# Kernel optimization log

Measured on AMD Instinct MI355X. Metric: run time of the kernel, lower is better.

The kernel has to match this reference:

```python
import jax, jax.numpy as jnp
import numpy as np

# Static hyperparams matching init_kwargs
KSIZE, STRIDE, PAD, DIL = 3, 2, 1, 1


def setup_inputs() -> dict:
    key = jax.random.key(0)
    k1, k2 = jax.random.split(key)
    B, H, W, Cin, Cout = 8, 128, 128, 128, 256
    feats = jax.random.normal(k1, (B * H * W, Cin), dtype=jnp.float32)
    weight = jax.random.normal(k2, (KSIZE * KSIZE, Cin, Cout), dtype=jnp.float32) * 0.05
    alpha_upper = jnp.ones((1,), dtype=jnp.float32)
    # dense grid coords [N, 3] = (batch, y, x), matching a dense image sparse tensor
    bb, yy, xx = np.meshgrid(np.arange(B), np.arange(H), np.arange(W), indexing='ij')
    coords = jnp.asarray(np.stack([bb, yy, xx], -1).reshape(-1, 3), dtype=jnp.int32)
    return {"feats": feats, "weight": weight, "alpha_upper": alpha_upper,
            "coords": coords, "H": H, "W": W, "B": B}


def _coord_ranges(H, W):
    # Faithful translation of WrappedMinkowskiStridedOperation.__init__ + forward
    # coordinate math, specialized to a dense grid (per-batch min=0, max=H-1/W-1).
    kernel_origin = DIL * ((KSIZE - 1) // 2) * (KSIZE % 2)
    dilated = DIL * (KSIZE - 1) + 1
    ks_off = kernel_origin - dilated + 1          # _kernel_start_offset
    ke_off = kernel_origin                        # _kernel_end_offset
    idx_start = kernel_origin - PAD               # _index_start_offset
    ranges = []
    for ext in (H, W):
        idx_end = (ext - 1) + kernel_origin + PAD - dilated + 2
        start = max(idx_start, (0 + ks_off - idx_start) // STRIDE * STRIDE + idx_start)
        end = min(idx_end, ((ext - 1 + ke_off - idx_start) // STRIDE + 1) * STRIDE + idx_start)
        ranges.append(np.arange(start, end, STRIDE))
    offsets = np.arange(KSIZE) * DIL - kernel_origin  # kernel region offsets
    return ranges[0], ranges[1], offsets, idx_start


def reference(feats, weight, alpha_upper, coords, H, W, B):
    Cin = feats.shape[1]
    Cout = weight.shape[-1]
    ys, xs, offs, idx_start = _coord_ranges(H, W)
    OH, OW = len(ys), len(xs)
    oy, ox = jnp.meshgrid(jnp.asarray(ys, jnp.int32), jnp.asarray(xs, jnp.int32), indexing='ij')
    dy, dx = np.meshgrid(offs, offs, indexing='ij')
    dy = jnp.asarray(dy.reshape(-1), jnp.int32)  # [kvol]
    dx = jnp.asarray(dx.reshape(-1), jnp.int32)
    ny = oy[None] + dy[:, None, None]            # [kvol, OH, OW]
    nx = ox[None] + dx[:, None, None]
    valid = (ny >= 0) & (ny < H) & (nx >= 0) & (nx < W)
    lin = jnp.clip(ny, 0, H - 1) * W + jnp.clip(nx, 0, W - 1)  # [kvol, OH, OW]
    feats3 = feats.reshape(B, H * W, Cin)
    gathered = feats3[:, lin]                    # [B, kvol, OH, OW, Cin]
    gathered = jnp.where(valid[None, ..., None], gathered, jnp.zeros((), feats.dtype))
    out = jnp.einsum('bkhwc,kcd->bhwd', gathered, weight)  # [B, OH, OW, Cout]
    out_feats = out.reshape(B * OH * OW, Cout)
    # output coordinates, remapped as in forward (shift by index_start, divide by stride)
    oc = jnp.stack([oy, ox], -1).reshape(-1, 2)  # [OH*OW, 2]
    oc = (oc - jnp.int32(idx_start)) // jnp.int32(STRIDE)
    oc = jnp.tile(oc, (B, 1))
    bcol = jnp.repeat(jnp.arange(B, dtype=jnp.int32), OH * OW)
    out_coords = jnp.concatenate([bcol[:, None], oc], axis=1)
    return out_feats, out_coords, alpha_upper
```

## Files before the change

### kernel.cpp

```cpp
#include <hip/hip_runtime.h>


#define OUT_FEATS_ELEMS (32768 * 256)
#define OUT_COORDS_OFF  OUT_FEATS_ELEMS
#define ALPHA_OFF       (OUT_FEATS_ELEMS + 32768 * 3)

typedef __bf16 v8bf __attribute__((ext_vector_type(8)));
typedef float  v4f  __attribute__((ext_vector_type(4)));

__device__ __forceinline__ unsigned short f2bf(float f) {
    union { float f; unsigned u; } v; v.f = f;
    return (unsigned short)((v.u + 0x7fffu + ((v.u >> 16) & 1u)) >> 16);
}

#define GLOAD_LDS16(SRC, DST)                                                  \
    __builtin_amdgcn_global_load_lds(                                          \
        (const __attribute__((address_space(1))) void*)(SRC),                  \
        (__attribute__((address_space(3))) void*)(DST), 16, 0, 0)

__global__ void conv_feats_kernel(const float4* __restrict__ f, ushort4* __restrict__ o) {
    int i = blockIdx.x * 256 + threadIdx.x;
    float4 v = f[i];
    ushort4 r;
    r.x = f2bf(v.x); r.y = f2bf(v.y); r.z = f2bf(v.z); r.w = f2bf(v.w);
    o[i] = r;
}

__global__ void wt_coords_kernel(const float* __restrict__ w, unsigned short* __restrict__ Bw,
                                 float* __restrict__ out, const float* __restrict__ alpha) {
    int cid = blockIdx.x * 256 + threadIdx.x;
    if (cid < 32768) {
        int b = cid >> 12, iy = (cid >> 6) & 63, ix = cid & 63;
        float* c = out + OUT_COORDS_OFF + (size_t)cid * 3;
        c[0] = (float)b; c[1] = (float)iy; c[2] = (float)ix;
        if (cid == 0) out[ALPHA_OFF] = alpha[0];
    }
    int ch  = cid & 7;
    int row = (cid >> 3) & 127;
    int t   = cid >> 10;
    int nb  = (t >= 18) ? 1 : 0;
    int ks  = t - 18 * nb;
    int tap = ks >> 1;
    int c0  = (ks & 1) << 6;
    int chp = ch ^ (row & 7);
    int n   = (nb << 7) + row;
    int kb  = (tap << 7) + c0 + (chp << 3);
    unsigned short r8[8];
#pragma unroll
    for (int j = 0; j < 8; ++j) r8[j] = f2bf(w[(size_t)(kb + j) * 256 + n]);
    *(uint4*)(Bw + (size_t)cid * 8) = *(const uint4*)r8;
}

__global__ void coords_alpha_kernel(float* __restrict__ out, const float* __restrict__ alpha) {
    int i = blockIdx.x * 256 + threadIdx.x;
    int b = i >> 12, iy = (i >> 6) & 63, ix = i & 63;
    float* c = out + OUT_COORDS_OFF + (size_t)i * 3;
    c[0] = (float)b; c[1] = (float)iy; c[2] = (float)ix;
    if (i == 0) out[ALPHA_OFF] = alpha[0];
}

__global__ __launch_bounds__(256, 2) void gemm_conv_kernel(
    const unsigned short* __restrict__ F,
    const unsigned short* __restrict__ Bw,
    float* __restrict__ out)
{
    __shared__ unsigned short At[128 * 64];
    __shared__ unsigned short Bs[128 * 64];

    const int tid  = threadIdx.x;
    const int nb   = blockIdx.x;
    const int n0   = nb << 7;
    const int m0   = (int)blockIdx.y << 7;
    const int bb   = (int)blockIdx.y >> 5;
    const int iy0  = ((int)blockIdx.y << 1) & 63;

    const int lane = tid & 63, wave = tid >> 6;
    const int wr   = (wave >> 1) << 6;
    const int wc   = (wave & 1) << 6;
    const int l15  = lane & 15, quad = lane >> 4;

    const int sr   = lane >> 3;
    const int ch   = lane & 7;
    const int chp  = ch ^ sr;
    const int iy_w = iy0 + (wave >> 1);
    const int ixb  = ((wave & 1) << 5) + sr;
    const long rowA0 = (long)bb << 14;

    const unsigned short* bsrc0 = Bw + (((size_t)nb * 18 * 1024) + ((size_t)wave << 8) + lane) * 8;
    unsigned short* adst0 = At + (wave << 11);
    unsigned short* bdst0 = Bs + (wave << 11);

    const int swz0 = (quad ^ (l15 & 7)) << 3;
    const int swz1 = ((4 + quad) ^ (l15 & 7)) << 3;

    v4f acc[4][4];
#pragma unroll
    for (int i = 0; i < 4; i++)
#pragma unroll
        for (int j = 0; j < 4; j++) acc[i][j] = (v4f)(0.0f);

    for (int ks = 0; ks < 18; ++ks) {
        const int tap = ks >> 1;
        const int c0  = (ks & 1) << 6;
        const int dy  = tap / 3 - 1;
        const int dx  = tap % 3 - 1;

        const int  ny = (iy_w << 1) + dy;
        const bool vy = (unsigned)ny < 128u;
        const long prow = rowA0 + ((long)ny << 7);

        __syncthreads();
#pragma unroll
        for (int it = 0; it < 4; ++it) {
            int nx = ((ixb + (it << 3)) << 1) + dx;
            bool v = vy & ((unsigned)nx < 128u);
            if (v) {
                const unsigned short* asrc = F + ((prow + nx) << 7) + c0 + (chp << 3);
                GLOAD_LDS16(asrc, adst0 + (it << 9));
            } else {
                uint4 z; z.x = 0u; z.y = 0u; z.z = 0u; z.w = 0u;
                *(uint4*)(At + (((wave << 5) + (it << 3) + sr) << 6) + (ch << 3)) = z;
            }
            GLOAD_LDS16(bsrc0 + (size_t)ks * 8192 + (it << 9), bdst0 + (it << 9));
        }
        __syncthreads();

        v8bf a0[4], a1[4], b0[4], b1[4];
#pragma unroll
        for (int i = 0; i < 4; i++) {
            const unsigned short* p = At + ((wr + (i << 4) + l15) << 6);
            a0[i] = *(const v8bf*)(p + swz0);
            a1[i] = *(const v8bf*)(p + swz1);
        }
#pragma unroll
        for (int j = 0; j < 4; j++) {
            const unsigned short* p = Bs + ((wc + (j << 4) + l15) << 6);
            b0[j] = *(const v8bf*)(p + swz0);
            b1[j] = *(const v8bf*)(p + swz1);
        }
#pragma unroll
        for (int i = 0; i < 4; i++)
#pragma unroll
            for (int j = 0; j < 4; j++) {
                acc[i][j] = __builtin_amdgcn_mfma_f32_16x16x32_bf16(a0[i], b0[j], acc[i][j], 0, 0, 0);
                acc[i][j] = __builtin_amdgcn_mfma_f32_16x16x32_bf16(a1[i], b1[j], acc[i][j], 0, 0, 0);
            }
    }

#pragma unroll
    for (int i = 0; i < 4; i++) {
        int mrow = m0 + wr + (i << 4) + (quad << 2);
#pragma unroll
        for (int j = 0; j < 4; j++) {
            int nn = n0 + wc + (j << 4) + l15;
#pragma unroll
            for (int r = 0; r < 4; r++)
                out[(size_t)(mrow + r) * 256 + nn] = acc[i][j][r];
        }
    }
}

__global__ void naive_conv_kernel(const float* __restrict__ feats,
                                  const float* __restrict__ w,
                                  float* __restrict__ out) {
    int m = blockIdx.x;
    int n = threadIdx.x;
    int bb = m >> 12, iy = (m >> 6) & 63, ix = m & 63;
    float acc = 0.f;
    for (int tap = 0; tap < 9; ++tap) {
        int ny = 2 * iy + tap / 3 - 1;
        int nx = 2 * ix + tap % 3 - 1;
        if ((unsigned)ny < 128u && (unsigned)nx < 128u) {
            const float* fr = feats + ((size_t)((bb << 14) + (ny << 7) + nx) << 7);
            const float* wr = w + tap * 32768 + n;
            for (int c = 0; c < 128; ++c) acc += fr[c] * wr[c * 256];
        }
    }
    out[(size_t)m * 256 + n] = acc;
}

extern "C" void kernel_launch(void* const* d_in, const int* in_sizes, int n_in,
                              void* d_out, int out_size, void* d_ws, size_t ws_size,
                              hipStream_t stream) {
    const float* feats  = (const float*)d_in[0];
    const float* weight = (const float*)d_in[1];
    const float* alpha  = (const float*)d_in[2];
    float* out = (float*)d_out;

    const size_t NEED = (size_t)16777216 * 2 + (size_t)2 * 18 * 1024 * 16;
    if (ws_size >= NEED) {
        unsigned short* Fb = (unsigned short*)d_ws;
        unsigned short* Bw = Fb + 16777216;
        conv_feats_kernel<<<16384, 256, 0, stream>>>((const float4*)feats, (ushort4*)Fb);
        wt_coords_kernel<<<144, 256, 0, stream>>>(weight, Bw, out, alpha);
        gemm_conv_kernel<<<dim3(2, 256), 256, 0, stream>>>(Fb, Bw, out);
    } else {
        coords_alpha_kernel<<<128, 256, 0, stream>>>(out, alpha);
        naive_conv_kernel<<<32768, 256, 0, stream>>>(feats, weight, out);
    }
}
```

Baseline: 145.7 us.

## Use 32x32x16 bf16 MFMA with full-tap K=128 tiles and 1D grid

```diff
diff --git a/kernel.cpp b/kernel.cpp
--- a/kernel.cpp
+++ b/kernel.cpp
@@ -5,8 +5,8 @@
 #define OUT_COORDS_OFF  OUT_FEATS_ELEMS
 #define ALPHA_OFF       (OUT_FEATS_ELEMS + 32768 * 3)
 
-typedef __bf16 v8bf __attribute__((ext_vector_type(8)));
-typedef float  v4f  __attribute__((ext_vector_type(4)));
+typedef __bf16 v8bf  __attribute__((ext_vector_type(8)));
+typedef float  v16f  __attribute__((ext_vector_type(16)));
 
 __device__ __forceinline__ unsigned short f2bf(float f) {
     union { float f; unsigned u; } v; v.f = f;
@@ -35,16 +35,14 @@
         c[0] = (float)b; c[1] = (float)iy; c[2] = (float)ix;
         if (cid == 0) out[ALPHA_OFF] = alpha[0];
     }
-    int ch  = cid & 7;
-    int row = (cid >> 3) & 127;
-    int t   = cid >> 10;
-    int nb  = (t >= 18) ? 1 : 0;
-    int ks  = t - 18 * nb;
-    int tap = ks >> 1;
-    int c0  = (ks & 1) << 6;
-    int chp = ch ^ (row & 7);
+    int ch  = cid & 15;
+    int row = (cid >> 4) & 127;
+    int t   = cid >> 11;
+    int nb  = (t >= 9) ? 1 : 0;
+    int tap = t - 9 * nb;
+    int cl  = ch ^ (row & 15);
     int n   = (nb << 7) + row;
-    int kb  = (tap << 7) + c0 + (chp << 3);
+    int kb  = (tap << 7) + (cl << 3);
     unsigned short r8[8];
 #pragma unroll
     for (int j = 0; j < 8; ++j) r8[j] = f2bf(w[(size_t)(kb + j) * 256 + n]);
@@ -64,100 +62,95 @@
     const unsigned short* __restrict__ Bw,
     float* __restrict__ out)
 {
-    __shared__ unsigned short At[128 * 64];
-    __shared__ unsigned short Bs[128 * 64];
+    __shared__ unsigned short At[128 * 128];
+    __shared__ unsigned short Bs[128 * 128];
 
     const int tid  = threadIdx.x;
-    const int nb   = blockIdx.x;
+    const int bid  = blockIdx.x;
+    const int my   = bid & 255;
+    const int nb   = bid >> 8;
     const int n0   = nb << 7;
-    const int m0   = (int)blockIdx.y << 7;
-    const int bb   = (int)blockIdx.y >> 5;
-    const int iy0  = ((int)blockIdx.y << 1) & 63;
+    const int m0   = my << 7;
+    const int bb   = my >> 5;
+    const int iy0  = (my << 1) & 63;
 
     const int lane = tid & 63, wave = tid >> 6;
-    const int wr   = (wave >> 1) << 6;
-    const int wc   = (wave & 1) << 6;
-    const int l15  = lane & 15, quad = lane >> 4;
+    const int wm   = (wave >> 1) << 6;
+    const int wn   = (wave & 1) << 6;
+    const int l31  = lane & 31;
+    const int hh   = lane >> 5;
+    const int xorm = lane & 15;
 
-    const int sr   = lane >> 3;
-    const int ch   = lane & 7;
-    const int chp  = ch ^ sr;
-    const int iy_w = iy0 + (wave >> 1);
-    const int ixb  = ((wave & 1) << 5) + sr;
+    const int srow4 = lane >> 4;
     const long rowA0 = (long)bb << 14;
+    const unsigned short* bimg = Bw + ((size_t)(nb * 9) << 14) + ((size_t)wave << 12) + ((size_t)lane << 3);
+    unsigned short* adst0 = At + (wave << 12);
+    unsigned short* bdst0 = Bs + (wave << 12);
 
-    const unsigned short* bsrc0 = Bw + (((size_t)nb * 18 * 1024) + ((size_t)wave << 8) + lane) * 8;
-    unsigned short* adst0 = At + (wave << 11);
-    unsigned short* bdst0 = Bs + (wave << 11);
+    v16f acc[2][2];
+#pragma unroll
+    for (int i = 0; i < 2; i++)
+#pragma unroll
+        for (int j = 0; j < 2; j++) acc[i][j] = (v16f)(0.0f);
 
-    const int swz0 = (quad ^ (l15 & 7)) << 3;
-    const int swz1 = ((4 + quad) ^ (l15 & 7)) << 3;
-
-    v4f acc[4][4];
-#pragma unroll
-    for (int i = 0; i < 4; i++)
-#pragma unroll
-        for (int j = 0; j < 4; j++) acc[i][j] = (v4f)(0.0f);
-
-    for (int ks = 0; ks < 18; ++ks) {
-        const int tap = ks >> 1;
-        const int c0  = (ks & 1) << 6;
-        const int dy  = tap / 3 - 1;
-        const int dx  = tap % 3 - 1;
-
-        const int  ny = (iy_w << 1) + dy;
-        const bool vy = (unsigned)ny < 128u;
-        const long prow = rowA0 + ((long)ny << 7);
+    for (int tap = 0; tap < 9; ++tap) {
+        const int dy = tap / 3 - 1;
+        const int dx = tap % 3 - 1;
 
         __syncthreads();
 #pragma unroll
-        for (int it = 0; it < 4; ++it) {
-            int nx = ((ixb + (it << 3)) << 1) + dx;
-            bool v = vy & ((unsigned)nx < 128u);
-            if (v) {
-                const unsigned short* asrc = F + ((prow + nx) << 7) + c0 + (chp << 3);
+        for (int it = 0; it < 8; ++it) {
+            const int region = (wave << 3) + it;
+            const int row    = (region << 2) + srow4;
+            const int iyl = row >> 6, ix = row & 63;
+            const int ny  = ((iy0 + iyl) << 1) + dy;
+            const int nx  = (ix << 1) + dx;
+            const int chp = xorm ^ (row & 15);
+            if (((unsigned)ny < 128u) & ((unsigned)nx < 128u)) {
+                const unsigned short* asrc =
+                    F + ((rowA0 + ((long)ny << 7) + nx) << 7) + (chp << 3);
                 GLOAD_LDS16(asrc, adst0 + (it << 9));
             } else {
                 uint4 z; z.x = 0u; z.y = 0u; z.z = 0u; z.w = 0u;
-                *(uint4*)(At + (((wave << 5) + (it << 3) + sr) << 6) + (ch << 3)) = z;
+                *(uint4*)(At + (region << 9) + (lane << 3)) = z;
             }
-            GLOAD_LDS16(bsrc0 + (size_t)ks * 8192 + (it << 9), bdst0 + (it << 9));
+            GLOAD_LDS16(bimg + ((size_t)tap << 14) + (it << 9), bdst0 + (it << 9));
         }
         __syncthreads();
 
-        v8bf a0[4], a1[4], b0[4], b1[4];
 #pragma unroll
-        for (int i = 0; i < 4; i++) {
-            const unsigned short* p = At + ((wr + (i << 4) + l15) << 6);
-            a0[i] = *(const v8bf*)(p + swz0);
-            a1[i] = *(const v8bf*)(p + swz1);
+        for (int seg = 0; seg < 8; ++seg) {
+            v8bf a[2], b[2];
+            const int c = ((seg << 1) + hh) ^ xorm;
+#pragma unroll
+            for (int i = 0; i < 2; i++) {
+                const int row = wm + (i << 5) + l31;
+                a[i] = *(const v8bf*)(At + (row << 7) + (c << 3));
+            }
+#pragma unroll
+            for (int j = 0; j < 2; j++) {
+                const int row = wn + (j << 5) + l31;
+                b[j] = *(const v8bf*)(Bs + (row << 7) + (c << 3));
+            }
+#pragma unroll
+            for (int i = 0; i < 2; i++)
+#pragma unroll
+                for (int j = 0; j < 2; j++)
+                    acc[i][j] = __builtin_amdgcn_mfma_f32_32x32x16_bf16(a[i], b[j], acc[i][j], 0, 0, 0);
         }
-#pragma unroll
-        for (int j = 0; j < 4; j++) {
-            const unsigned short* p = Bs + ((wc + (j << 4) + l15) << 6);
-            b0[j] = *(const v8bf*)(p + swz0);
-            b1[j] = *(const v8bf*)(p + swz1);
-        }
-#pragma unroll
-        for (int i = 0; i < 4; i++)
-#pragma unroll
-            for (int j = 0; j < 4; j++) {
-                acc[i][j] = __builtin_amdgcn_mfma_f32_16x16x32_bf16(a0[i], b0[j], acc[i][j], 0, 0, 0);
-                acc[i][j] = __builtin_amdgcn_mfma_f32_16x16x32_bf16(a1[i], b1[j], acc[i][j], 0, 0, 0);
-            }
     }
 
 #pragma unroll
-    for (int i = 0; i < 4; i++) {
-        int mrow = m0 + wr + (i << 4) + (quad << 2);
+    for (int i = 0; i < 2; i++)
 #pragma unroll
-        for (int j = 0; j < 4; j++) {
-            int nn = n0 + wc + (j << 4) + l15;
+        for (int j = 0; j < 2; j++) {
+            const int gcol = n0 + wn + (j << 5) + l31;
 #pragma unroll
-            for (int r = 0; r < 4; r++)
-                out[(size_t)(mrow + r) * 256 + nn] = acc[i][j][r];
+            for (int r = 0; r < 16; ++r) {
+                const int grow = m0 + wm + (i << 5) + (r & 3) + ((r >> 2) << 3) + (hh << 2);
+                out[(size_t)grow * 256 + gcol] = acc[i][j][r];
+            }
         }
-    }
 }
 
 __global__ void naive_conv_kernel(const float* __restrict__ feats,
@@ -187,13 +180,13 @@
     const float* alpha  = (const float*)d_in[2];
     float* out = (float*)d_out;
 
-    const size_t NEED = (size_t)16777216 * 2 + (size_t)2 * 18 * 1024 * 16;
+    const size_t NEED = (size_t)16777216 * 2 + (size_t)18 * 16384 * 2;
     if (ws_size >= NEED) {
         unsigned short* Fb = (unsigned short*)d_ws;
         unsigned short* Bw = Fb + 16777216;
         conv_feats_kernel<<<16384, 256, 0, stream>>>((const float4*)feats, (ushort4*)Fb);
         wt_coords_kernel<<<144, 256, 0, stream>>>(weight, Bw, out, alpha);
-        gemm_conv_kernel<<<dim3(2, 256), 256, 0, stream>>>(Fb, Bw, out);
+        gemm_conv_kernel<<<512, 256, 0, stream>>>(Fb, Bw, out);
     } else {
         coords_alpha_kernel<<<128, 256, 0, stream>>>(out, alpha);
         naive_conv_kernel<<<32768, 256, 0, stream>>>(feats, weight, out);
```

Measured after the change: 145.1 us. Within noise of the previous version (-0.4%).
